# Performance work log

Measured on AMD Instinct MI355X. Metric: run time of the kernel, lower is better.

Reference implementation:

```python
import jax, jax.numpy as jnp
import numpy as np

B, N, E, D, AD = 8, 1000, 4, 64, 32  # batch, n_node, n_edge_types, state_dim, annotation_dim
W_SCALE = 0.02  # matches normal_(0.0, 0.02) init


def setup_inputs() -> dict:
    key = jax.random.key(0)
    ks = jax.random.split(key, 10)
    return {
        "prop_state": jax.random.normal(ks[0], (B, N, D), jnp.float32),
        "annotation": jax.random.normal(ks[1], (B, N, AD), jnp.float32),
        "A": jax.random.uniform(ks[2], (B, N, 2 * N * E), jnp.float32),
        "W_in": W_SCALE * jax.random.normal(ks[3], (E, D, D), jnp.float32),
        "W_out": W_SCALE * jax.random.normal(ks[4], (E, D, D), jnp.float32),
        "W_r": W_SCALE * jax.random.normal(ks[5], (D, 3 * D), jnp.float32),
        "W_z": W_SCALE * jax.random.normal(ks[6], (D, 3 * D), jnp.float32),
        "W_h": W_SCALE * jax.random.normal(ks[7], (D, 3 * D), jnp.float32),
        "Wo1": W_SCALE * jax.random.normal(ks[8], (D, D + AD), jnp.float32),
        "Wo2": W_SCALE * jax.random.normal(ks[9], (1, D), jnp.float32),
    }


def _propagate(state, A_in, A_out, W_in, W_out, W_r, W_z, W_h):
    b, n, d = state.shape
    e = W_in.shape[0]
    # per-edge-type linear transforms (torch Linear: y = x @ W.T), batched over edge types
    # layout matches torch: stack over e then transpose(0,1) -> [b, e, n, d] -> [b, e*n, d]
    s_in = jnp.einsum('bnd,efd->benf', state, W_in).reshape(b, e * n, d)
    s_out = jnp.einsum('bnd,efd->benf', state, W_out).reshape(b, e * n, d)
    a_in = jnp.matmul(A_in, s_in)    # [b, n, d]
    a_out = jnp.matmul(A_out, s_out)  # [b, n, d]
    a = jnp.concatenate([a_in, a_out, state], axis=2)  # [b, n, 3d]
    r = jax.nn.sigmoid(a @ W_r.T)
    z = jax.nn.sigmoid(a @ W_z.T)
    joined = jnp.concatenate([a_in, a_out, r * state], axis=2)
    h_hat = jnp.tanh(joined @ W_h.T)
    return (1.0 - z) * state + z * h_hat


def reference(prop_state, annotation, A, W_in, W_out, W_r, W_z, W_h, Wo1, Wo2):
    n = prop_state.shape[1]
    e = W_in.shape[0]
    ne = n * e
    A_in, A_out = A[:, :, :ne], A[:, :, ne:]
    # exactly two propagation steps (n_steps_flag path in the original)
    s1 = _propagate(prop_state, A_in, A_out, W_in, W_out, W_r, W_z, W_h)
    s2 = _propagate(s1, A_in, A_out, W_in, W_out, W_r, W_z, W_h)
    join_state = jnp.concatenate([s2, annotation], axis=2)  # [b, n, d+ad]
    out = jnp.tanh(join_state @ Wo1.T) @ Wo2.T  # [b, n, 1]
    return out.sum(axis=2)  # [b, n]
```

## Files before the change

### kernel.cpp

```cpp
#include <hip/hip_runtime.h>


typedef float  f32x4_t  __attribute__((ext_vector_type(4)));
typedef __bf16 bf16x8_t __attribute__((ext_vector_type(8)));
typedef __bf16 bf16x4_t __attribute__((ext_vector_type(4)));

#define MFMA16(a, b, c) __builtin_amdgcn_mfma_f32_16x16x32_bf16((a), (b), (c), 0, 0, 0)

static constexpr int kN     = 1000;
static constexpr int kD     = 64;
static constexpr int kAD    = 32;
static constexpr int kP     = 8000 * 64;
static constexpr int kPl    = 5;

__device__ __forceinline__ float4 ld4(const float* p) {
    return *reinterpret_cast<const float4*>(p);
}

__device__ __forceinline__ bf16x8_t cvt8(float4 a, float4 b) {
    bf16x8_t r;
    r[0] = (__bf16)a.x; r[1] = (__bf16)a.y; r[2] = (__bf16)a.z; r[3] = (__bf16)a.w;
    r[4] = (__bf16)b.x; r[5] = (__bf16)b.y; r[6] = (__bf16)b.z; r[7] = (__bf16)b.w;
    return r;
}

__device__ __forceinline__ bf16x8_t sum5p(const float* p) {
    float s0 = 0.f, s1 = 0.f, s2 = 0.f, s3 = 0.f;
    float s4 = 0.f, s5 = 0.f, s6 = 0.f, s7 = 0.f;
    #pragma unroll
    for (int pl = 0; pl < kPl; ++pl) {
        const float4 a0 = ld4(p + (size_t)pl * kP);
        const float4 a1 = ld4(p + (size_t)pl * kP + 4);
        s0 += a0.x; s1 += a0.y; s2 += a0.z; s3 += a0.w;
        s4 += a1.x; s5 += a1.y; s6 += a1.z; s7 += a1.w;
    }
    bf16x8_t r;
    r[0] = (__bf16)s0; r[1] = (__bf16)s1; r[2] = (__bf16)s2; r[3] = (__bf16)s3;
    r[4] = (__bf16)s4; r[5] = (__bf16)s5; r[6] = (__bf16)s6; r[7] = (__bf16)s7;
    return r;
}

__device__ __forceinline__ float sigm(float x) {
    x = fminf(fmaxf(x, -30.f), 30.f);
    return 1.0f / (1.0f + __expf(-x));
}

__device__ __forceinline__ float fast_tanh(float x) {
    x = fminf(fmaxf(x, -15.f), 15.f);
    const float e = __expf(-2.0f * x);
    return (1.0f - e) / (1.0f + e);
}

__global__ __launch_bounds__(256) void precompute_swt(
    const float* __restrict__ state,
    const float* __restrict__ W_in,
    const float* __restrict__ W_out,
    __bf16* __restrict__ SWTfrag)
{
    const int bx = blockIdx.x;
    const int jt = bx & 15;
    const int e  = (bx >> 4) & 3;
    const int h  = (bx >> 6) & 1;
    const int b  = bx >> 7;
    const float* W = (h ? W_out : W_in) + e * kD * kD;

    const int tid  = threadIdx.x;
    const int w    = tid >> 6;
    const int lane = tid & 63;
    const int m    = lane & 15;
    const int q    = lane >> 4;

    __shared__ __bf16 T[64][72];

    const int  jj    = jt * 64 + w * 16 + m;
    const bool valid = (jj < kN);
    const float* srow = state + ((size_t)b * kN + (valid ? jj : kN - 1)) * kD + q * 8;
    float4 a0 = ld4(srow),      a1 = ld4(srow + 4);
    float4 a2 = ld4(srow + 32), a3 = ld4(srow + 36);
    if (!valid) {
        a0 = make_float4(0.f, 0.f, 0.f, 0.f); a1 = a0; a2 = a0; a3 = a0;
    }
    const bf16x8_t af0 = cvt8(a0, a1);
    const bf16x8_t af1 = cvt8(a2, a3);

    #pragma unroll
    for (int c = 0; c < 4; ++c) {
        const int f = c * 16 + m;
        const float* wrow = W + f * kD + q * 8;
        const bf16x8_t bf0 = cvt8(ld4(wrow),      ld4(wrow + 4));
        const bf16x8_t bf1 = cvt8(ld4(wrow + 32), ld4(wrow + 36));
        f32x4_t acc = {0.f, 0.f, 0.f, 0.f};
        acc = MFMA16(af0, bf0, acc);
        acc = MFMA16(af1, bf1, acc);
        const int j0 = w * 16 + q * 4;
        bf16x4_t v;
        v[0] = (__bf16)acc[0]; v[1] = (__bf16)acc[1];
        v[2] = (__bf16)acc[2]; v[3] = (__bf16)acc[3];
        *reinterpret_cast<bf16x4_t*>(&T[f][j0]) = v;
    }
    __syncthreads();

    const int bh = b * 2 + h;
    #pragma unroll
    for (int rep = 0; rep < 2; ++rep) {
        const int m2 = tid & 15;
        const int cc = (tid >> 4) & 3;
        const int ol = (tid >> 6) + rep * 4;
        const int j0 = jt * 64 + ol * 8;
        if (j0 < kN) {
            const int jg = e * kN + j0;
            const int s  = jg >> 5;
            const int qq = (jg >> 3) & 3;
            const uint4 v = *reinterpret_cast<uint4*>(&T[cc * 16 + m2][ol * 8]);
            const size_t el = ((((size_t)bh * 125 + s) * 4 + cc) * 64 + qq * 16 + m2) * 8;
            *reinterpret_cast<uint4*>((__bf16*)SWTfrag + el) = v;
        }
    }
}

__global__ __launch_bounds__(256, 4) void fused_mm1(
    const float* __restrict__ A,
    const __bf16* __restrict__ SWTfrag,
    __bf16* __restrict__ Afrag,
    float* __restrict__ a_in_p,
    float* __restrict__ a_out_p)
{
    const int bx   = blockIdx.x;
    const int tile = bx & 15;
    const int rest = bx >> 4;
    const int kseg = rest % 5;
    const int rhb  = rest / 5;
    const int h    = rhb & 1;
    const int b    = rhb >> 1;

    const int t    = threadIdx.x;
    const int wv   = t >> 6;
    const int lane = t & 63;
    const int m    = lane & 15;
    const int q    = lane >> 4;

    __shared__ __bf16 L[2][64][136];

    const float* Abase = A + (size_t)b * kN * 8000 + h * 4000;
    const int bh = b * 2 + h;

    f32x4_t acc0 = {0.f, 0.f, 0.f, 0.f};
    f32x4_t acc1 = {0.f, 0.f, 0.f, 0.f};
    f32x4_t acc2 = {0.f, 0.f, 0.f, 0.f};
    f32x4_t acc3 = {0.f, 0.f, 0.f, 0.f};

    const __bf16* pBbase = SWTfrag + (size_t)bh * 125 * 2048 + (size_t)lane * 8;
    __bf16* pAout = Afrag +
        ((((size_t)(bh * 64 + tile * 4 + wv)) * 125) * 64 + lane) * 8;

    float4 ra[4][2];

    auto load_chunk = [&](int c, bool tail) {
        const int kabs = kseg * 800 + c * 128;
        #pragma unroll
        for (int p = 0; p < 4; ++p) {
            if (p == 0 || !tail) {
                const int idx = p * 256 + t;
                const int r   = tail ? (t >> 2) : (idx >> 4);
                const int c8  = tail ? (t & 3)  : (idx & 15);
                int i = tile * 64 + r;
                if (i >= kN) i = kN - 1;
                const float* src = Abase + (size_t)i * 8000 + kabs + c8 * 8;
                ra[p][0] = ld4(src);
                ra[p][1] = ld4(src + 4);
            }
        }
    };
    auto write_chunk = [&](int buf, bool tail) {
        #pragma unroll
        for (int p = 0; p < 4; ++p) {
            if (p == 0 || !tail) {
                const int idx = p * 256 + t;
                const int r   = tail ? (t >> 2) : (idx >> 4);
                const int c8  = tail ? (t & 3)  : (idx & 15);
                *reinterpret_cast<bf16x8_t*>(&L[buf][r][c8 * 8]) =
                    cvt8(ra[p][0], ra[p][1]);
            }
        }
    };
    auto compute_chunk = [&](int c, int nst, int buf) {
        #pragma unroll
        for (int sp = 0; sp < 4; ++sp) {
            if (sp < nst) {
                const int s = kseg * 25 + c * 4 + sp;
                const bf16x8_t af =
                    *reinterpret_cast<const bf16x8_t*>(&L[buf][wv * 16 + m][sp * 32 + q * 8]);
                *reinterpret_cast<bf16x8_t*>(pAout + (size_t)s * 512) = af;

                const __bf16* pB = pBbase + (size_t)s * 2048;
                const bf16x8_t b0 = *(const bf16x8_t*)(pB);
                const bf16x8_t b1 = *(const bf16x8_t*)(pB + 512);
                const bf16x8_t b2 = *(const bf16x8_t*)(pB + 1024);
                const bf16x8_t b3 = *(const bf16x8_t*)(pB + 1536);
                acc0 = MFMA16(af, b0, acc0);
                acc1 = MFMA16(af, b1, acc1);
                acc2 = MFMA16(af, b2, acc2);
                acc3 = MFMA16(af, b3, acc3);
            }
        }
    };

    load_chunk(0, false);
    write_chunk(0, false);
    __syncthreads();
    load_chunk(1, false);

    #pragma unroll 1
    for (int c = 0; c < 6; ++c) {
        compute_chunk(c, 4, c & 1);
        write_chunk((c + 1) & 1, c + 1 == 6);
        __syncthreads();
        if (c < 5)
            load_chunk(c + 2, c + 2 == 6);
    }
    compute_chunk(6, 1, 0);

    float* dst = (h ? a_out_p : a_in_p) + (size_t)kseg * kP + (size_t)b * kN * kD;
    const int i0 = tile * 64 + wv * 16 + q * 4;
    #pragma unroll
    for (int r = 0; r < 4; ++r) {
        const int i = i0 + r;
        if (i < kN) {
            float* drow = dst + (size_t)i * kD + m;
            drow[0]  = acc0[r];
            drow[16] = acc1[r];
            drow[32] = acc2[r];
            drow[48] = acc3[r];
        }
    }
}

__global__ __launch_bounds__(256, 4) void big_mm_f(
    const __bf16* __restrict__ Afrag,
    const __bf16* __restrict__ SWTfrag,
    float* __restrict__ a_in_p,
    float* __restrict__ a_out_p)
{
    const int bx   = blockIdx.x;
    const int tile = bx & 15;
    const int h    = (bx >> 4) & 1;
    const int b    = (bx >> 5) & 7;
    const int ksp  = bx >> 8;
    const int t    = threadIdx.x;
    const int wv   = t >> 6;
    const int lane = t & 63;
    const int m    = lane & 15;
    const int q    = lane >> 4;

    const int s0 = ksp * 25;
    const int ns = 25;

    const int bh = b * 2 + h;
    const __bf16* pA = Afrag +
        ((((size_t)(bh * 64 + tile * 4 + wv)) * 125 + s0) * 64 + lane) * 8;
    const __bf16* pB = SWTfrag +
        (((size_t)bh * 125 + s0) * 4 * 64) * 8 + (size_t)lane * 8;

    f32x4_t acc0 = {0.f, 0.f, 0.f, 0.f};
    f32x4_t acc1 = {0.f, 0.f, 0.f, 0.f};
    f32x4_t acc2 = {0.f, 0.f, 0.f, 0.f};
    f32x4_t acc3 = {0.f, 0.f, 0.f, 0.f};

    bf16x8_t cA  = *(const bf16x8_t*)(pA);
    bf16x8_t cB0 = *(const bf16x8_t*)(pB);
    bf16x8_t cB1 = *(const bf16x8_t*)(pB + 512);
    bf16x8_t cB2 = *(const bf16x8_t*)(pB + 1024);
    bf16x8_t cB3 = *(const bf16x8_t*)(pB + 1536);

    for (int s = 0; s < ns; ++s) {
        const int adv = (s + 1 < ns) ? 1 : 0;
        pA += adv * 512;
        pB += adv * 2048;
        const bf16x8_t nA  = *(const bf16x8_t*)(pA);
        const bf16x8_t nB0 = *(const bf16x8_t*)(pB);
        const bf16x8_t nB1 = *(const bf16x8_t*)(pB + 512);
        const bf16x8_t nB2 = *(const bf16x8_t*)(pB + 1024);
        const bf16x8_t nB3 = *(const bf16x8_t*)(pB + 1536);

        acc0 = MFMA16(cA, cB0, acc0);
        acc1 = MFMA16(cA, cB1, acc1);
        acc2 = MFMA16(cA, cB2, acc2);
        acc3 = MFMA16(cA, cB3, acc3);

        cA = nA; cB0 = nB0; cB1 = nB1; cB2 = nB2; cB3 = nB3;
    }

    float* dst = (h ? a_out_p : a_in_p) + (size_t)ksp * kP + (size_t)b * kN * kD;
    const int i0 = tile * 64 + wv * 16 + q * 4;
    #pragma unroll
    for (int r = 0; r < 4; ++r) {
        const int i = i0 + r;
        if (i < kN) {
            float* drow = dst + (size_t)i * kD + m;
            drow[0]  = acc0[r];
            drow[16] = acc1[r];
            drow[32] = acc2[r];
            drow[48] = acc3[r];
        }
    }
}

__global__ __launch_bounds__(256, 2) void gating(
    const float* __restrict__ a_in_p,
    const float* __restrict__ a_out_p,
    const float* __restrict__ state,
    const float* __restrict__ W_r,
    const float* __restrict__ W_z,
    const float* __restrict__ W_h,
    float* __restrict__ s_next,
    const float* __restrict__ ann,
    const float* __restrict__ Wo1,
    const float* __restrict__ Wo2,
    float* __restrict__ out,
    const int step)
{
    const int i0   = blockIdx.x * 16;
    const int tid  = threadIdx.x;
    const int c    = tid >> 6;
    const int lane = tid & 63;
    const int m    = lane & 15;
    const int q    = lane >> 4;
    const int f    = c * 16 + m;

    __shared__ __bf16 TL[16][72];
    __shared__ float  Osum[4][16];

    const size_t rowA = (size_t)(i0 + m);

    bf16x8_t xf[6];
    {
        const float* p = a_in_p + rowA * kD + q * 8;
        xf[0] = sum5p(p);
        xf[1] = sum5p(p + 32);
        p = a_out_p + rowA * kD + q * 8;
        xf[2] = sum5p(p);
        xf[3] = sum5p(p + 32);
        p = state + rowA * kD + q * 8;
        xf[4] = cvt8(ld4(p),      ld4(p + 4));
        xf[5] = cvt8(ld4(p + 32), ld4(p + 36));
    }

    f32x4_t accr = {0.f, 0.f, 0.f, 0.f};
    f32x4_t accz = {0.f, 0.f, 0.f, 0.f};
    f32x4_t acch = {0.f, 0.f, 0.f, 0.f};

    const float* wr = W_r + f * 192 + q * 8;
    const float* wz = W_z + f * 192 + q * 8;
    const float* wh = W_h + f * 192 + q * 8;
    #pragma unroll
    for (int kc = 0; kc < 6; ++kc) {
        accr = MFMA16(xf[kc], cvt8(ld4(wr + kc * 32), ld4(wr + kc * 32 + 4)), accr);
        accz = MFMA16(xf[kc], cvt8(ld4(wz + kc * 32), ld4(wz + kc * 32 + 4)), accz);
        if (kc < 4)
            acch = MFMA16(xf[kc], cvt8(ld4(wh + kc * 32), ld4(wh + kc * 32 + 4)), acch);
    }

    float sC[4];
    #pragma unroll
    for (int r = 0; r < 4; ++r)
        sC[r] = state[(size_t)(i0 + q * 4 + r) * kD + f];

    #pragma unroll
    for (int r = 0; r < 4; ++r)
        TL[q * 4 + r][f] = (__bf16)(sigm(accr[r]) * sC[r]);
    __syncthreads();
    const bf16x8_t rs0 = *(const bf16x8_t*)&TL[m][q * 8];
    const bf16x8_t rs1 = *(const bf16x8_t*)&TL[m][32 + q * 8];

    const float* wh3 = W_h + f * 192 + 128 + q * 8;
    acch = MFMA16(rs0, cvt8(ld4(wh3),      ld4(wh3 + 4)),  acch);
    acch = MFMA16(rs1, cvt8(ld4(wh3 + 32), ld4(wh3 + 36)), acch);

    float ns[4];
    #pragma unroll
    for (int r = 0; r < 4; ++r) {
        const float zv = sigm(accz[r]);
        ns[r] = (1.f - zv) * sC[r] + zv * fast_tanh(acch[r]);
    }

    if (step == 1) {
        #pragma unroll
        for (int r = 0; r < 4; ++r)
            s_next[(size_t)(i0 + q * 4 + r) * kD + f] = ns[r];
    } else {
        __syncthreads();
        #pragma unroll
        for (int r = 0; r < 4; ++r)
            TL[q * 4 + r][f] = (__bf16)ns[r];
        __syncthreads();
        const bf16x8_t j0 = *(const bf16x8_t*)&TL[m][q * 8];
        const bf16x8_t j1 = *(const bf16x8_t*)&TL[m][32 + q * 8];
        const float* ap = ann + rowA * kAD + q * 8;
        const bf16x8_t j2 = cvt8(ld4(ap), ld4(ap + 4));

        f32x4_t acco = {0.f, 0.f, 0.f, 0.f};
        const float* wo = Wo1 + (size_t)f * 96 + q * 8;
        acco = MFMA16(j0, cvt8(ld4(wo),      ld4(wo + 4)),  acco);
        acco = MFMA16(j1, cvt8(ld4(wo + 32), ld4(wo + 36)), acco);
        acco = MFMA16(j2, cvt8(ld4(wo + 64), ld4(wo + 68)), acco);

        const float w2 = Wo2[f];
        float vs[4];
        #pragma unroll
        for (int r = 0; r < 4; ++r)
            vs[r] = fast_tanh(acco[r]) * w2;
        #pragma unroll
        for (int off = 1; off <= 8; off <<= 1) {
            #pragma unroll
            for (int r = 0; r < 4; ++r)
                vs[r] += __shfl_xor(vs[r], off, 64);
        }
        if (m == 0) {
            #pragma unroll
            for (int r = 0; r < 4; ++r)
                Osum[c][q * 4 + r] = vs[r];
        }
        __syncthreads();
        if (tid < 16)
            out[i0 + tid] = Osum[0][tid] + Osum[1][tid] + Osum[2][tid] + Osum[3][tid];
    }
}

extern "C" void kernel_launch(void* const* d_in, const int* in_sizes, int n_in,
                              void* d_out, int out_size, void* d_ws, size_t ws_size,
                              hipStream_t stream) {
    (void)in_sizes; (void)n_in; (void)out_size; (void)ws_size;

    const float* prop_state = (const float*)d_in[0];
    const float* annotation = (const float*)d_in[1];
    const float* A          = (const float*)d_in[2];
    const float* W_in       = (const float*)d_in[3];
    const float* W_out      = (const float*)d_in[4];
    const float* W_r        = (const float*)d_in[5];
    const float* W_z        = (const float*)d_in[6];
    const float* W_h        = (const float*)d_in[7];
    const float* Wo1        = (const float*)d_in[8];
    const float* Wo2        = (const float*)d_in[9];
    float* out = (float*)d_out;

    char* ws = (char*)d_ws;
    __bf16* Afrag   = (__bf16*)(ws);
    __bf16* SWTfrag = (__bf16*)(ws + 131072000);
    float*  a_in_p  = (float*)(ws + 139264000);
    float*  a_out_p = (float*)(ws + 149504000);
    float*  s1      = (float*)(ws + 159744000);

    precompute_swt<<<1024, 256, 0, stream>>>(prop_state, W_in, W_out, SWTfrag);
    fused_mm1<<<1280, 256, 0, stream>>>(A, SWTfrag, Afrag, a_in_p, a_out_p);
    gating<<<500, 256, 0, stream>>>(a_in_p, a_out_p, prop_state, W_r, W_z, W_h,
                                    s1, nullptr, nullptr, nullptr, nullptr, 1);
    precompute_swt<<<1024, 256, 0, stream>>>(s1, W_in, W_out, SWTfrag);
    big_mm_f<<<1280, 256, 0, stream>>>(Afrag, SWTfrag, a_in_p, a_out_p);
    gating<<<500, 256, 0, stream>>>(a_in_p, a_out_p, s1, W_r, W_z, W_h,
                                    nullptr, annotation, Wo1, Wo2, out, 2);
}
```

Before: 495.7 us.

## Store partial sums in bf16 and fuse step-two SWT precompute into gating

Measured after the change: 481.7 us. 2.8% less time.

```diff
diff --git a/kernel.cpp b/kernel.cpp
--- a/kernel.cpp
+++ b/kernel.cpp
@@ -7,11 +7,11 @@
 
 #define MFMA16(a, b, c) __builtin_amdgcn_mfma_f32_16x16x32_bf16((a), (b), (c), 0, 0, 0)
 
-static constexpr int kN     = 1000;
-static constexpr int kD     = 64;
-static constexpr int kAD    = 32;
-static constexpr int kP     = 8000 * 64;
-static constexpr int kPl    = 5;
+static constexpr int kN   = 1000;
+static constexpr int kD   = 64;
+static constexpr int kAD  = 32;
+static constexpr int kPb  = 8000 * 64;
+static constexpr int kPl  = 5;
 
 __device__ __forceinline__ float4 ld4(const float* p) {
     return *reinterpret_cast<const float4*>(p);
@@ -24,15 +24,14 @@
     return r;
 }
 
-__device__ __forceinline__ bf16x8_t sum5p(const float* p) {
+__device__ __forceinline__ bf16x8_t sum5pb(const __bf16* p) {
     float s0 = 0.f, s1 = 0.f, s2 = 0.f, s3 = 0.f;
     float s4 = 0.f, s5 = 0.f, s6 = 0.f, s7 = 0.f;
     #pragma unroll
     for (int pl = 0; pl < kPl; ++pl) {
-        const float4 a0 = ld4(p + (size_t)pl * kP);
-        const float4 a1 = ld4(p + (size_t)pl * kP + 4);
-        s0 += a0.x; s1 += a0.y; s2 += a0.z; s3 += a0.w;
-        s4 += a1.x; s5 += a1.y; s6 += a1.z; s7 += a1.w;
+        const bf16x8_t v = *reinterpret_cast<const bf16x8_t*>(p + (size_t)pl * kPb);
+        s0 += (float)v[0]; s1 += (float)v[1]; s2 += (float)v[2]; s3 += (float)v[3];
+        s4 += (float)v[4]; s5 += (float)v[5]; s6 += (float)v[6]; s7 += (float)v[7];
     }
     bf16x8_t r;
     r[0] = (__bf16)s0; r[1] = (__bf16)s1; r[2] = (__bf16)s2; r[3] = (__bf16)s3;
@@ -122,8 +121,8 @@
     const float* __restrict__ A,
     const __bf16* __restrict__ SWTfrag,
     __bf16* __restrict__ Afrag,
-    float* __restrict__ a_in_p,
-    float* __restrict__ a_out_p)
+    __bf16* __restrict__ a_in_p,
+    __bf16* __restrict__ a_out_p)
 {
     const int bx   = blockIdx.x;
     const int tile = bx & 15;
@@ -220,17 +219,25 @@
     }
     compute_chunk(6, 1, 0);
 
-    float* dst = (h ? a_out_p : a_in_p) + (size_t)kseg * kP + (size_t)b * kN * kD;
-    const int i0 = tile * 64 + wv * 16 + q * 4;
+    __bf16* Tw = &L[0][wv * 16][64];
     #pragma unroll
     for (int r = 0; r < 4; ++r) {
-        const int i = i0 + r;
+        const int row = q * 4 + r;
+        Tw[row * 136 + m]      = (__bf16)acc0[r];
+        Tw[row * 136 + 16 + m] = (__bf16)acc1[r];
+        Tw[row * 136 + 32 + m] = (__bf16)acc2[r];
+        Tw[row * 136 + 48 + m] = (__bf16)acc3[r];
+    }
+    __bf16* dstb = (h ? a_out_p : a_in_p) + (size_t)kseg * kPb + (size_t)b * kN * kD;
+    const int ibase = tile * 64 + wv * 16;
+    #pragma unroll
+    for (int p2 = 0; p2 < 2; ++p2) {
+        const int jr = p2 * 8 + (lane >> 3);
+        const int c8 = lane & 7;
+        const int i  = ibase + jr;
         if (i < kN) {
-            float* drow = dst + (size_t)i * kD + m;
-            drow[0]  = acc0[r];
-            drow[16] = acc1[r];
-            drow[32] = acc2[r];
-            drow[48] = acc3[r];
+            const bf16x8_t v = *reinterpret_cast<const bf16x8_t*>(&Tw[jr * 136 + c8 * 8]);
+            *reinterpret_cast<bf16x8_t*>(dstb + (size_t)i * kD + c8 * 8) = v;
         }
     }
 }
@@ -238,8 +245,8 @@
 __global__ __launch_bounds__(256, 4) void big_mm_f(
     const __bf16* __restrict__ Afrag,
     const __bf16* __restrict__ SWTfrag,
-    float* __restrict__ a_in_p,
-    float* __restrict__ a_out_p)
+    __bf16* __restrict__ a_in_p,
+    __bf16* __restrict__ a_out_p)
 {
     const int bx   = blockIdx.x;
     const int tile = bx & 15;
@@ -252,6 +259,8 @@
     const int m    = lane & 15;
     const int q    = lane >> 4;
 
+    __shared__ __bf16 T[4][16][72];
+
     const int s0 = ksp * 25;
     const int ns = 25;
 
@@ -290,29 +299,39 @@
         cA = nA; cB0 = nB0; cB1 = nB1; cB2 = nB2; cB3 = nB3;
     }
 
-    float* dst = (h ? a_out_p : a_in_p) + (size_t)ksp * kP + (size_t)b * kN * kD;
-    const int i0 = tile * 64 + wv * 16 + q * 4;
     #pragma unroll
     for (int r = 0; r < 4; ++r) {
-        const int i = i0 + r;
+        const int row = q * 4 + r;
+        T[wv][row][m]      = (__bf16)acc0[r];
+        T[wv][row][16 + m] = (__bf16)acc1[r];
+        T[wv][row][32 + m] = (__bf16)acc2[r];
+        T[wv][row][48 + m] = (__bf16)acc3[r];
+    }
+    __bf16* dstb = (h ? a_out_p : a_in_p) + (size_t)ksp * kPb + (size_t)b * kN * kD;
+    const int ibase = tile * 64 + wv * 16;
+    #pragma unroll
+    for (int p2 = 0; p2 < 2; ++p2) {
+        const int jr = p2 * 8 + (lane >> 3);
+        const int c8 = lane & 7;
+        const int i  = ibase + jr;
         if (i < kN) {
-            float* drow = dst + (size_t)i * kD + m;
-            drow[0]  = acc0[r];
-            drow[16] = acc1[r];
-            drow[32] = acc2[r];
-            drow[48] = acc3[r];
+            const bf16x8_t v = *reinterpret_cast<const bf16x8_t*>(&T[wv][jr][c8 * 8]);
+            *reinterpret_cast<bf16x8_t*>(dstb + (size_t)i * kD + c8 * 8) = v;
         }
     }
 }
 
 __global__ __launch_bounds__(256, 2) void gating(
-    const float* __restrict__ a_in_p,
-    const float* __restrict__ a_out_p,
+    const __bf16* __restrict__ a_in_p,
+    const __bf16* __restrict__ a_out_p,
     const float* __restrict__ state,
     const float* __restrict__ W_r,
     const float* __restrict__ W_z,
     const float* __restrict__ W_h,
     float* __restrict__ s_next,
+    const float* __restrict__ W_in,
+    const float* __restrict__ W_out,
+    __bf16* __restrict__ SWTfrag,
     const float* __restrict__ ann,
     const float* __restrict__ Wo1,
     const float* __restrict__ Wo2,
@@ -334,15 +353,15 @@
 
     bf16x8_t xf[6];
     {
-        const float* p = a_in_p + rowA * kD + q * 8;
-        xf[0] = sum5p(p);
-        xf[1] = sum5p(p + 32);
+        const __bf16* p = a_in_p + rowA * kD + q * 8;
+        xf[0] = sum5pb(p);
+        xf[1] = sum5pb(p + 32);
         p = a_out_p + rowA * kD + q * 8;
-        xf[2] = sum5p(p);
-        xf[3] = sum5p(p + 32);
-        p = state + rowA * kD + q * 8;
-        xf[4] = cvt8(ld4(p),      ld4(p + 4));
-        xf[5] = cvt8(ld4(p + 32), ld4(p + 36));
+        xf[2] = sum5pb(p);
+        xf[3] = sum5pb(p + 32);
+        const float* ps = state + rowA * kD + q * 8;
+        xf[4] = cvt8(ld4(ps),      ld4(ps + 4));
+        xf[5] = cvt8(ld4(ps + 32), ld4(ps + 36));
     }
 
     f32x4_t accr = {0.f, 0.f, 0.f, 0.f};
@@ -387,6 +406,47 @@
         #pragma unroll
         for (int r = 0; r < 4; ++r)
             s_next[(size_t)(i0 + q * 4 + r) * kD + f] = ns[r];
+
+        __syncthreads();
+        #pragma unroll
+        for (int r = 0; r < 4; ++r)
+            TL[q * 4 + r][f] = (__bf16)ns[r];
+        __syncthreads();
+        const bf16x8_t sj0 = *(const bf16x8_t*)&TL[m][q * 8];
+        const bf16x8_t sj1 = *(const bf16x8_t*)&TL[m][32 + q * 8];
+
+        const int row0 = i0 + q * 4;
+        const int bb   = row0 / 1000;
+        const int jj0  = row0 - bb * 1000;
+
+        #pragma unroll
+        for (int u = 0; u < 2; ++u) {
+            const int eh = c * 2 + u;
+            const int hh = eh >> 2;
+            const int ee = eh & 3;
+            const float* W = (hh ? W_out : W_in) + ee * kD * kD;
+            const int jg0 = ee * 1000 + jj0;
+            const int s   = jg0 >> 5;
+            const int qq  = (jg0 >> 3) & 3;
+            const int jo  = jg0 & 7;
+            const int bh2 = bb * 2 + hh;
+            #pragma unroll
+            for (int fg = 0; fg < 4; ++fg) {
+                const int fp = fg * 16 + m;
+                const float* wrow = W + fp * kD + q * 8;
+                const bf16x8_t bf0 = cvt8(ld4(wrow),      ld4(wrow + 4));
+                const bf16x8_t bf1 = cvt8(ld4(wrow + 32), ld4(wrow + 36));
+                f32x4_t acc = {0.f, 0.f, 0.f, 0.f};
+                acc = MFMA16(sj0, bf0, acc);
+                acc = MFMA16(sj1, bf1, acc);
+                bf16x4_t v;
+                v[0] = (__bf16)acc[0]; v[1] = (__bf16)acc[1];
+                v[2] = (__bf16)acc[2]; v[3] = (__bf16)acc[3];
+                const size_t el =
+                    ((((size_t)bh2 * 125 + s) * 4 + fg) * 64 + qq * 16 + m) * 8 + jo;
+                *reinterpret_cast<bf16x4_t*>(SWTfrag + el) = v;
+            }
+        }
     } else {
         __syncthreads();
         #pragma unroll
@@ -446,16 +506,17 @@
     char* ws = (char*)d_ws;
     __bf16* Afrag   = (__bf16*)(ws);
     __bf16* SWTfrag = (__bf16*)(ws + 131072000);
-    float*  a_in_p  = (float*)(ws + 139264000);
-    float*  a_out_p = (float*)(ws + 149504000);
-    float*  s1      = (float*)(ws + 159744000);
+    __bf16* a_in_p  = (__bf16*)(ws + 139264000);
+    __bf16* a_out_p = (__bf16*)(ws + 144384000);
+    float*  s1      = (float*)(ws + 149504000);
 
     precompute_swt<<<1024, 256, 0, stream>>>(prop_state, W_in, W_out, SWTfrag);
     fused_mm1<<<1280, 256, 0, stream>>>(A, SWTfrag, Afrag, a_in_p, a_out_p);
     gating<<<500, 256, 0, stream>>>(a_in_p, a_out_p, prop_state, W_r, W_z, W_h,
-                                    s1, nullptr, nullptr, nullptr, nullptr, 1);
-    precompute_swt<<<1024, 256, 0, stream>>>(s1, W_in, W_out, SWTfrag);
+                                    s1, W_in, W_out, SWTfrag,
+                                    nullptr, nullptr, nullptr, nullptr, 1);
     big_mm_f<<<1280, 256, 0, stream>>>(Afrag, SWTfrag, a_in_p, a_out_p);
     gating<<<500, 256, 0, stream>>>(a_in_p, a_out_p, s1, W_r, W_z, W_h,
-                                    nullptr, annotation, Wo1, Wo2, out, 2);
-}
+                                    nullptr, nullptr, nullptr, nullptr,
+                                    annotation, Wo1, Wo2, out, 2);
+}
```
